# Kernel tuning notes

Hardware: AMD Instinct MI355X
Metric: run time of the kernel (lower is better)

Reference implementation:

```python
import jax, jax.numpy as jnp
import numpy as np

B, T, D, H = 2, 2048, 1024, 16
DH = D // H  # 64


def setup_inputs() -> dict:
    key = jax.random.key(0)
    k1, k2, k3 = jax.random.split(key, 3)
    x = jax.random.normal(k1, (B, T, D), dtype=jnp.float32)
    # torch nn.Linear(d, 3d, bias=False): y = x @ W.T; we store W already transposed as [in, out]
    Wqkv = jax.random.normal(k2, (D, 3 * D), dtype=jnp.float32) * (1.0 / np.sqrt(D))
    Wproj = jax.random.normal(k3, (D, D), dtype=jnp.float32) * (1.0 / np.sqrt(D))
    return {"x": x, "Wqkv": Wqkv, "Wproj": Wproj}


def reference(x, Wqkv, Wproj):
    Bx, Tx, C = x.shape
    qkv = x @ Wqkv                                   # [B,T,3C]
    q, k, v = jnp.split(qkv, 3, axis=-1)
    def rs(t):
        return t.reshape(Bx, Tx, H, DH).transpose(0, 2, 1, 3)  # [B,H,T,DH]
    q, k, v = rs(q), rs(k), rs(v)
    scale = 1.0 / jnp.sqrt(jnp.asarray(DH, dtype=x.dtype))
    att = jnp.einsum('bhqd,bhkd->bhqk', q, k) * scale          # [B,H,T,T]
    causal = jnp.tril(jnp.ones((Tx, Tx), dtype=bool))
    att = jnp.where(causal[None, None, :, :], att, jnp.asarray(-jnp.inf, dtype=att.dtype))
    att = jax.nn.softmax(att, axis=-1)
    out = jnp.einsum('bhqk,bhkd->bhqd', att, v)                # [B,H,T,DH]
    out = out.transpose(0, 2, 1, 3).reshape(Bx, Tx, C)         # [B,T,C]
    return out @ Wproj
```

## Files before the change

### kernel.cpp

```cpp
#include <hip/hip_runtime.h>
#include <hip/hip_bf16.h>

#define BB 2
#define TT 2048
#define DD 1024
#define HH 16
#define MM (BB*TT)
#define N3 (3*DD)
#define QKW 2048

typedef __attribute__((ext_vector_type(8))) short short8;
typedef __attribute__((ext_vector_type(4))) float f32x4;
typedef __attribute__((ext_vector_type(16))) float f32x16;

#define ZERO16 (f32x16){0,0,0,0,0,0,0,0,0,0,0,0,0,0,0,0}

#define GLDS16(g, l) __builtin_amdgcn_global_load_lds( \
    (const __attribute__((address_space(1))) void*)(g), \
    (__attribute__((address_space(3))) void*)(l), 16, 0, 0)

__device__ __forceinline__ unsigned short f2bf(float f) {
    union { float f; unsigned u; } v; v.f = f;
    unsigned r = v.u + 0x7FFFu + ((v.u >> 16) & 1u);
    return (unsigned short)(r >> 16);
}

__device__ __forceinline__ unsigned cvt_pk_bf16(float lo, float hi) {
    unsigned r;
    asm("v_cvt_pk_bf16_f32 %0, %1, %2" : "=v"(r) : "v"(lo), "v"(hi));
    return r;
}

__device__ __forceinline__ float fast_exp2(float x) {
    float r;
    asm("v_exp_f32 %0, %1" : "=v"(r) : "v"(x));
    return r;
}
__device__ __forceinline__ float fast_rcp(float x) {
    float r;
    asm("v_rcp_f32 %0, %1" : "=v"(r) : "v"(x));
    return r;
}

__global__ void prep_kernel(const float* __restrict__ x,
                            const float* __restrict__ Wqkv,
                            const float* __restrict__ Wproj,
                            unsigned short* __restrict__ xb,
                            unsigned short* __restrict__ wqkvt,
                            unsigned short* __restrict__ wprojt) {
    __shared__ float tile[32][33];
    const int bid = blockIdx.x;
    const int tx = threadIdx.x, ty = threadIdx.y;
    if (bid < 4096) {
        const float* src;
        unsigned short* dst;
        int rows, cols, c0, r0;
        if (bid < 3072) {
            src = Wqkv; dst = wqkvt; rows = DD; cols = N3;
            c0 = (bid % 96) * 32; r0 = (bid / 96) * 32;
        } else {
            src = Wproj; dst = wprojt; rows = DD; cols = DD;
            int b2 = bid - 3072;
            c0 = (b2 & 31) * 32; r0 = (b2 >> 5) * 32;
        }
#pragma unroll
        for (int i = 0; i < 4; i++) {
            int r = ty + i * 8;
            tile[r][tx] = src[(size_t)(r0 + r) * cols + c0 + tx];
        }
        __syncthreads();
#pragma unroll
        for (int i = 0; i < 4; i++) {
            int r = ty + i * 8;
            dst[(size_t)(c0 + r) * rows + r0 + tx] = f2bf(tile[tx][r]);
        }
    } else {
        const int t = ty * 32 + tx;
        int i = (bid - 4096) * 256 + t;
#pragma unroll
        for (int k = 0; k < 2; k++, i += 262144) {
            const float4* s = reinterpret_cast<const float4*>(x) + (size_t)i * 2;
            float4 a = s[0], b = s[1];
            unsigned short r[8] = {f2bf(a.x), f2bf(a.y), f2bf(a.z), f2bf(a.w),
                                   f2bf(b.x), f2bf(b.y), f2bf(b.z), f2bf(b.w)};
            *reinterpret_cast<uint4*>(xb + (size_t)i * 8) = *reinterpret_cast<uint4*>(r);
        }
    }
}

__global__ __launch_bounds__(512, 2)
void gemm256_qkv(const unsigned short* __restrict__ A,
                 const unsigned short* __restrict__ Bt,
                 unsigned short* __restrict__ qkv2,
                 unsigned short* __restrict__ Vout,
                 float scale) {
    __shared__ unsigned short Al[2][2][128][64];
    __shared__ unsigned short Bl[2][192][64];

    const int id = blockIdx.y * 16 + blockIdx.x;
    const int swzid = (id & 7) * 32 + (id >> 3);
    const int tm = (swzid >> 4) * 256, tn = (swzid & 15) * 192;
    const int t = threadIdx.x, w = t >> 6, l = t & 63;
    const int wm = w >> 2, wn = w & 3;
    const int lo = l & 15, hi = l >> 4;
    const int srow = l >> 3;
    const int sg = (l & 7) ^ srow;

    f32x4 acc[8][3];
#pragma unroll
    for (int i = 0; i < 8; i++)
#pragma unroll
        for (int j = 0; j < 3; j++) acc[i][j] = (f32x4){0.f, 0.f, 0.f, 0.f};

    const unsigned short* Abase = A + (size_t)(tm + w * 16 + srow) * 1024 + sg * 8;
    const unsigned short* Bbase = Bt + (size_t)(tn + w * 24 + srow) * 1024 + sg * 8;

#define STG_A(KT, H) { \
    GLDS16(Abase + (size_t)(H) * 128 * 1024 + ((KT) & 15) * 64, &Al[(KT) & 1][H][w * 16][0]); \
    GLDS16(Abase + (size_t)(H) * 128 * 1024 + 8 * 1024 + ((KT) & 15) * 64, &Al[(KT) & 1][H][w * 16 + 8][0]); }
#define STG_B(KT) { \
    GLDS16(Bbase + ((KT) & 15) * 64, &Bl[(KT) & 1][w * 24][0]); \
    GLDS16(Bbase + (size_t)8 * 1024 + ((KT) & 15) * 64, &Bl[(KT) & 1][w * 24 + 8][0]); \
    GLDS16(Bbase + (size_t)16 * 1024 + ((KT) & 15) * 64, &Bl[(KT) & 1][w * 24 + 16][0]); }

#define LOAD_A(AFR, KP, MH) { \
    const char* ab = (const char*)&Al[KP][wm][0][0]; \
    _Pragma("unroll") \
    for (int fi = 0; fi < 4; fi++) \
    _Pragma("unroll") \
    for (int ks = 0; ks < 2; ks++) \
        AFR[fi][ks] = *reinterpret_cast<const short8*>( \
            ab + ((MH) * 64 + fi * 16 + lo) * 128 + (((ks * 4 + hi) ^ (lo & 7)) << 4)); }
#define LOAD_B(BFR, KP) { \
    const char* bb = (const char*)&Bl[KP][0][0]; \
    _Pragma("unroll") \
    for (int fj = 0; fj < 3; fj++) \
    _Pragma("unroll") \
    for (int ks = 0; ks < 2; ks++) \
        BFR[fj][ks] = *reinterpret_cast<const short8*>( \
            bb + (wn * 48 + fj * 16 + lo) * 128 + (((ks * 4 + hi) ^ (lo & 7)) << 4)); }

#define MFMA24(MH, AFR, BFR) { \
    _Pragma("unroll") \
    for (int ks = 0; ks < 2; ks++) \
    _Pragma("unroll") \
    for (int fi = 0; fi < 4; fi++) \
    _Pragma("unroll") \
    for (int fj = 0; fj < 3; fj++) \
        acc[(MH) * 4 + fi][fj] = __builtin_amdgcn_mfma_f32_16x16x32_bf16( \
            AFR[fi][ks], BFR[fj][ks], acc[(MH) * 4 + fi][fj], 0, 0, 0); }

#define BAR __builtin_amdgcn_s_barrier()
#define LGKM0 asm volatile("s_waitcnt lgkmcnt(0)")
#define SP1 __builtin_amdgcn_s_setprio(1)
#define SP0 __builtin_amdgcn_s_setprio(0)

    STG_A(0, 0); STG_A(0, 1); STG_B(0); STG_B(1);
    asm volatile("s_waitcnt vmcnt(3)");
    BAR;

    for (int i = 0; i < 8; i++) {
        const int kt = 2 * i;
        short8 AF[4][2], BF[3][2];
        LOAD_A(AF, 0, 0); LOAD_B(BF, 0);
        STG_A(kt + 1, 0); STG_A(kt + 1, 1);
        BAR; LGKM0; SP1; MFMA24(0, AF, BF); SP0; BAR;
        LOAD_A(AF, 0, 1);
        STG_B(kt + 2);
        BAR; LGKM0; SP1; MFMA24(1, AF, BF); SP0;
        asm volatile("s_waitcnt vmcnt(3)");
        BAR;
        LOAD_A(AF, 1, 0); LOAD_B(BF, 1);
        STG_A(kt + 2, 0); STG_A(kt + 2, 1);
        BAR; LGKM0; SP1; MFMA24(0, AF, BF); SP0; BAR;
        LOAD_A(AF, 1, 1);
        STG_B(kt + 3);
        BAR; LGKM0; SP1; MFMA24(1, AF, BF); SP0;
        asm volatile("s_waitcnt vmcnt(3)");
        BAR;
    }

#pragma unroll
    for (int i = 0; i < 8; i++)
#pragma unroll
        for (int j = 0; j < 3; j++) {
            const int col = tn + wn * 48 + j * 16 + lo;
            const int row0 = tm + wm * 128 + i * 16 + hi * 4;
            if (col < 2 * DD) {
                float s = (col < DD) ? scale : 1.0f;
#pragma unroll
                for (int r = 0; r < 4; r++)
                    qkv2[(size_t)(row0 + r) * QKW + col] = f2bf(acc[i][j][r] * s);
            } else {
                unsigned short pk[4];
#pragma unroll
                for (int r = 0; r < 4; r++) pk[r] = f2bf(acc[i][j][r]);
                *reinterpret_cast<uint2*>(&Vout[(size_t)(col - 2 * DD) * MM + row0]) =
                    *reinterpret_cast<uint2*>(pk);
            }
        }
#undef STG_A
#undef STG_B
#undef LOAD_A
#undef LOAD_B
#undef MFMA24
#undef BAR
#undef LGKM0
#undef SP1
#undef SP0
}

__global__ __launch_bounds__(256, 4)
void gemm_proj(const unsigned short* __restrict__ A,
               const unsigned short* __restrict__ Bt,
               float* __restrict__ Cout) {
    __shared__ unsigned short As[128][64];
    __shared__ unsigned short Bs[64][64];
    const int nbx = 16;
    const int id = blockIdx.y * nbx + blockIdx.x;
    const int cpx = 512 >> 3;
    const int swz = (id & 7) * cpx + (id >> 3);
    const int tm = (swz / nbx) * 128, tn = (swz % nbx) * 64;
    const int t = threadIdx.x;
    const int w = t >> 6, lane = t & 63, lo = lane & 15, hi = lane >> 4;
    const int wr = w >> 1, wc = w & 1;

    f32x4 acc[4][2];
#pragma unroll
    for (int i = 0; i < 4; i++)
#pragma unroll
        for (int j = 0; j < 2; j++) acc[i][j] = (f32x4){0.f, 0.f, 0.f, 0.f};

    const int sr8 = lane >> 3;
    const int scol = (lane & 7) * 8;
    const unsigned short* ga = &A[(size_t)(tm + w * 32 + sr8) * 1024 + scol];
    const unsigned short* gb = &Bt[(size_t)(tn + w * 16 + sr8) * 1024 + scol];

    for (int k0 = 0; k0 < 1024; k0 += 64) {
        __syncthreads();
#pragma unroll
        for (int i = 0; i < 4; i++)
            GLDS16(ga + (size_t)(i * 8) * 1024 + k0, &As[w * 32 + i * 8][0]);
#pragma unroll
        for (int i = 0; i < 2; i++)
            GLDS16(gb + (size_t)(i * 8) * 1024 + k0, &Bs[w * 16 + i * 8][0]);
        __syncthreads();

        short8 af[4][2], bf[2][2];
#pragma unroll
        for (int i = 0; i < 4; i++)
#pragma unroll
            for (int ks = 0; ks < 2; ks++)
                af[i][ks] = *reinterpret_cast<const short8*>(&As[wr * 64 + i * 16 + lo][ks * 32 + hi * 8]);
#pragma unroll
        for (int j = 0; j < 2; j++)
#pragma unroll
            for (int ks = 0; ks < 2; ks++)
                bf[j][ks] = *reinterpret_cast<const short8*>(&Bs[wc * 32 + j * 16 + lo][ks * 32 + hi * 8]);
#pragma unroll
        for (int ks = 0; ks < 2; ks++)
#pragma unroll
            for (int i = 0; i < 4; i++)
#pragma unroll
                for (int j = 0; j < 2; j++)
                    acc[i][j] = __builtin_amdgcn_mfma_f32_16x16x32_bf16(af[i][ks], bf[j][ks], acc[i][j], 0, 0, 0);
    }
#pragma unroll
    for (int i = 0; i < 4; i++)
#pragma unroll
        for (int j = 0; j < 2; j++) {
            const int col = tn + wc * 32 + j * 16 + lo;
            const int row0 = tm + wr * 64 + i * 16 + hi * 4;
#pragma unroll
            for (int r = 0; r < 4; r++)
                Cout[(size_t)(row0 + r) * DD + col] = acc[i][j][r];
        }
}

struct AttnState {
    f32x16 o0, o1, lD;
};

__device__ __forceinline__ void attn_full_tile(
        const char* kbase, const char* vbase, const short8* bq, short8 ones1,
        AttnState& st, int sw4, int ql, int hi8, bool domask, int kvb, int qg) {
    short8 ak0[4], ak1[4];
#pragma unroll
    for (int ks = 0; ks < 4; ks++) {
        ak0[ks] = *reinterpret_cast<const short8*>(kbase + ql * 128 + (((ks * 2 + hi8) << 4) ^ sw4));
        ak1[ks] = *reinterpret_cast<const short8*>(kbase + (32 + ql) * 128 + (((ks * 2 + hi8) << 4) ^ sw4));
    }
    f32x16 sa0 = ZERO16, sa1 = ZERO16;
    __builtin_amdgcn_s_setprio(1);
#pragma unroll
    for (int ks = 0; ks < 4; ks++) {
        sa0 = __builtin_amdgcn_mfma_f32_32x32x16_bf16(ak0[ks], bq[ks], sa0, 0, 0, 0);
        sa1 = __builtin_amdgcn_mfma_f32_32x32x16_bf16(ak1[ks], bq[ks], sa1, 0, 0, 0);
    }
    __builtin_amdgcn_s_setprio(0);
    if (domask) {
#pragma unroll
        for (int r = 0; r < 16; r++) {
            int crow = (r & 3) + 8 * (r >> 2) + 4 * hi8;
            if (kvb + crow > qg) sa0[r] = -1e30f;
            if (kvb + 32 + crow > qg) sa1[r] = -1e30f;
        }
    }
#pragma unroll
    for (int r = 0; r < 16; r++) sa0[r] = fast_exp2(sa0[r]);
#pragma unroll
    for (int r = 0; r < 16; r++) sa1[r] = fast_exp2(sa1[r]);

    unsigned a01 = cvt_pk_bf16(sa0[0], sa0[1]),  a23 = cvt_pk_bf16(sa0[2], sa0[3]);
    unsigned a45 = cvt_pk_bf16(sa0[4], sa0[5]),  a67 = cvt_pk_bf16(sa0[6], sa0[7]);
    asm("v_permlane32_swap_b32 %0, %1" : "+v"(a01), "+v"(a45));
    asm("v_permlane32_swap_b32 %0, %1" : "+v"(a23), "+v"(a67));
    unsigned b01 = cvt_pk_bf16(sa0[8], sa0[9]),  b23 = cvt_pk_bf16(sa0[10], sa0[11]);
    unsigned b45 = cvt_pk_bf16(sa0[12], sa0[13]), b67 = cvt_pk_bf16(sa0[14], sa0[15]);
    asm("v_permlane32_swap_b32 %0, %1" : "+v"(b01), "+v"(b45));
    asm("v_permlane32_swap_b32 %0, %1" : "+v"(b23), "+v"(b67));
    unsigned c01 = cvt_pk_bf16(sa1[0], sa1[1]),  c23 = cvt_pk_bf16(sa1[2], sa1[3]);
    unsigned c45 = cvt_pk_bf16(sa1[4], sa1[5]),  c67 = cvt_pk_bf16(sa1[6], sa1[7]);
    asm("v_permlane32_swap_b32 %0, %1" : "+v"(c01), "+v"(c45));
    asm("v_permlane32_swap_b32 %0, %1" : "+v"(c23), "+v"(c67));
    unsigned d01 = cvt_pk_bf16(sa1[8], sa1[9]),  d23 = cvt_pk_bf16(sa1[10], sa1[11]);
    unsigned d45 = cvt_pk_bf16(sa1[12], sa1[13]), d67 = cvt_pk_bf16(sa1[14], sa1[15]);
    asm("v_permlane32_swap_b32 %0, %1" : "+v"(d01), "+v"(d45));
    asm("v_permlane32_swap_b32 %0, %1" : "+v"(d23), "+v"(d67));
    union { unsigned u[4]; short8 s; } f0s0, f1s0, f0s1, f1s1;
    f0s0.u[0] = a01; f0s0.u[1] = a23; f0s0.u[2] = a45; f0s0.u[3] = a67;
    f1s0.u[0] = b01; f1s0.u[1] = b23; f1s0.u[2] = b45; f1s0.u[3] = b67;
    f0s1.u[0] = c01; f0s1.u[1] = c23; f0s1.u[2] = c45; f0s1.u[3] = c67;
    f1s1.u[0] = d01; f1s1.u[1] = d23; f1s1.u[2] = d45; f1s1.u[3] = d67;

    short8 bv00 = *reinterpret_cast<const short8*>(vbase + ql * 128 + (((0 + hi8) << 4) ^ sw4));
    short8 bv01 = *reinterpret_cast<const short8*>(vbase + ql * 128 + (((2 + hi8) << 4) ^ sw4));
    short8 bv02 = *reinterpret_cast<const short8*>(vbase + ql * 128 + (((4 + hi8) << 4) ^ sw4));
    short8 bv03 = *reinterpret_cast<const short8*>(vbase + ql * 128 + (((6 + hi8) << 4) ^ sw4));
    short8 bv10 = *reinterpret_cast<const short8*>(vbase + (32 + ql) * 128 + (((0 + hi8) << 4) ^ sw4));
    short8 bv11 = *reinterpret_cast<const short8*>(vbase + (32 + ql) * 128 + (((2 + hi8) << 4) ^ sw4));
    short8 bv12 = *reinterpret_cast<const short8*>(vbase + (32 + ql) * 128 + (((4 + hi8) << 4) ^ sw4));
    short8 bv13 = *reinterpret_cast<const short8*>(vbase + (32 + ql) * 128 + (((6 + hi8) << 4) ^ sw4));
    __builtin_amdgcn_s_setprio(1);
    st.lD = __builtin_amdgcn_mfma_f32_32x32x16_bf16(f0s0.s, ones1, st.lD, 0, 0, 0);
    st.lD = __builtin_amdgcn_mfma_f32_32x32x16_bf16(f1s0.s, ones1, st.lD, 0, 0, 0);
    st.lD = __builtin_amdgcn_mfma_f32_32x32x16_bf16(f0s1.s, ones1, st.lD, 0, 0, 0);
    st.lD = __builtin_amdgcn_mfma_f32_32x32x16_bf16(f1s1.s, ones1, st.lD, 0, 0, 0);
    st.o0 = __builtin_amdgcn_mfma_f32_32x32x16_bf16(f0s0.s, bv00, st.o0, 0, 0, 0);
    st.o1 = __builtin_amdgcn_mfma_f32_32x32x16_bf16(f0s0.s, bv10, st.o1, 0, 0, 0);
    st.o0 = __builtin_amdgcn_mfma_f32_32x32x16_bf16(f1s0.s, bv01, st.o0, 0, 0, 0);
    st.o1 = __builtin_amdgcn_mfma_f32_32x32x16_bf16(f1s0.s, bv11, st.o1, 0, 0, 0);
    st.o0 = __builtin_amdgcn_mfma_f32_32x32x16_bf16(f0s1.s, bv02, st.o0, 0, 0, 0);
    st.o1 = __builtin_amdgcn_mfma_f32_32x32x16_bf16(f0s1.s, bv12, st.o1, 0, 0, 0);
    st.o0 = __builtin_amdgcn_mfma_f32_32x32x16_bf16(f1s1.s, bv03, st.o0, 0, 0, 0);
    st.o1 = __builtin_amdgcn_mfma_f32_32x32x16_bf16(f1s1.s, bv13, st.o1, 0, 0, 0);
    __builtin_amdgcn_s_setprio(0);
}

__device__ __forceinline__ void attn_half_tile(
        const char* kbase, const char* vbase, const short8* bq, short8 ones1,
        AttnState& st, int sw4, int ql, int hi8, int sub, int kvb, int qg) {
    short8 ak[4];
#pragma unroll
    for (int ks = 0; ks < 4; ks++)
        ak[ks] = *reinterpret_cast<const short8*>(
            kbase + (sub * 32 + ql) * 128 + (((ks * 2 + hi8) << 4) ^ sw4));
    f32x16 sa = ZERO16;
#pragma unroll
    for (int ks = 0; ks < 4; ks++)
        sa = __builtin_amdgcn_mfma_f32_32x32x16_bf16(ak[ks], bq[ks], sa, 0, 0, 0);

#pragma unroll
    for (int r = 0; r < 16; r++) {
        int crow = (r & 3) + 8 * (r >> 2) + 4 * hi8;
        if (kvb + sub * 32 + crow > qg) sa[r] = -1e30f;
    }
#pragma unroll
    for (int r = 0; r < 16; r++) sa[r] = fast_exp2(sa[r]);

    unsigned a01 = cvt_pk_bf16(sa[0], sa[1]),  a23 = cvt_pk_bf16(sa[2], sa[3]);
    unsigned a45 = cvt_pk_bf16(sa[4], sa[5]),  a67 = cvt_pk_bf16(sa[6], sa[7]);
    asm("v_permlane32_swap_b32 %0, %1" : "+v"(a01), "+v"(a45));
    asm("v_permlane32_swap_b32 %0, %1" : "+v"(a23), "+v"(a67));
    unsigned b01 = cvt_pk_bf16(sa[8], sa[9]),  b23 = cvt_pk_bf16(sa[10], sa[11]);
    unsigned b45 = cvt_pk_bf16(sa[12], sa[13]), b67 = cvt_pk_bf16(sa[14], sa[15]);
    asm("v_permlane32_swap_b32 %0, %1" : "+v"(b01), "+v"(b45));
    asm("v_permlane32_swap_b32 %0, %1" : "+v"(b23), "+v"(b67));
    union { unsigned u[4]; short8 s; } f0, f1;
    f0.u[0] = a01; f0.u[1] = a23; f0.u[2] = a45; f0.u[3] = a67;
    f1.u[0] = b01; f1.u[1] = b23; f1.u[2] = b45; f1.u[3] = b67;

    st.lD = __builtin_amdgcn_mfma_f32_32x32x16_bf16(f0.s, ones1, st.lD, 0, 0, 0);
    st.lD = __builtin_amdgcn_mfma_f32_32x32x16_bf16(f1.s, ones1, st.lD, 0, 0, 0);

    short8 bv00 = *reinterpret_cast<const short8*>(vbase + ql * 128 + (((sub * 4 + 0 + hi8) << 4) ^ sw4));
    short8 bv01 = *reinterpret_cast<const short8*>(vbase + ql * 128 + (((sub * 4 + 2 + hi8) << 4) ^ sw4));
    short8 bv10 = *reinterpret_cast<const short8*>(vbase + (32 + ql) * 128 + (((sub * 4 + 0 + hi8) << 4) ^ sw4));
    short8 bv11 = *reinterpret_cast<const short8*>(vbase + (32 + ql) * 128 + (((sub * 4 + 2 + hi8) << 4) ^ sw4));
    st.o0 = __builtin_amdgcn_mfma_f32_32x32x16_bf16(f0.s, bv00, st.o0, 0, 0, 0);
    st.o1 = __builtin_amdgcn_mfma_f32_32x32x16_bf16(f0.s, bv10, st.o1, 0, 0, 0);
    st.o0 = __builtin_amdgcn_mfma_f32_32x32x16_bf16(f1.s, bv01, st.o0, 0, 0, 0);
    st.o1 = __builtin_amdgcn_mfma_f32_32x32x16_bf16(f1.s, bv11, st.o1, 0, 0, 0);
}

__global__ __launch_bounds__(256)
void attn_kernel(const unsigned short* __restrict__ qkv2,
                 const unsigned short* __restrict__ vtg,
                 unsigned short* __restrict__ outp) {
    __shared__ unsigned short Ks[4][64][64];
    __shared__ unsigned short Vt[4][64][64];

    const int b = blockIdx.z, h = blockIdx.x, p = blockIdx.y;
    const int qcl = p, qch = 31 - p;
    const int L = p + 1, Hn = 32 - p;
    const int NSTEP = 17;
    const int t = threadIdx.x;
    const int w = t >> 6, l = t & 63, ql = l & 31, hi8 = l >> 5;
    const int pr = w >> 1, rg = w & 1;
    const int q0h = qch * 64 + rg * 32;
    const int q0l = qcl * 64 + rg * 32;
    const int q0p = pr ? q0l : q0h;
    const unsigned short* base2 = qkv2 + (size_t)b * TT * QKW;

    short8 bq[4];
#pragma unroll
    for (int ks = 0; ks < 4; ks++)
        bq[ks] = *reinterpret_cast<const short8*>(
            &base2[(size_t)(q0p + ql) * QKW + h * 64 + ks * 16 + hi8 * 8]);

    AttnState st;
    st.o0 = ZERO16; st.o1 = ZERO16; st.lD = ZERO16;

    short8 ones1;
#pragma unroll
    for (int j = 0; j < 8; j++) ones1[j] = (short)0x3F80;

    const int krow = l >> 3;
    const int kc8 = (l & 7) ^ krow;
    const unsigned short* gk = &base2[(size_t)(w * 8 + krow) * QKW + DD + h * 64 + kc8 * 8];
    const unsigned short* gv = &vtg[(size_t)(h * 64 + w * 8 + krow) * MM + b * TT + kc8 * 8];

#define STAGE(TI) { \
    const int _s = (TI) & 3; \
    const size_t _kb = (size_t)(TI) * 64; \
    GLDS16(gk + _kb * QKW, &Ks[_s][w * 8][0]); \
    GLDS16(gk + (_kb + 32) * QKW, &Ks[_s][32 + w * 8][0]); \
    GLDS16(gv + _kb, &Vt[_s][w * 8][0]); \
    GLDS16(gv + (size_t)32 * MM + _kb, &Vt[_s][32 + w * 8][0]); }

#define WRITE_OUT(Q0) { \
    _Pragma("unroll") \
    for (int r = 0; r < 16; r++) { \
        int src = (r & 3) + 8 * (r >> 2) + 4 * hi8; \
        float inv = fast_rcp(st.lD[r]); \
        size_t off = (size_t)(b * TT + (Q0) + src) * DD + h * 64 + ql; \
        outp[off] = f2bf(st.o0[r] * inv); \
        outp[off + 32] = f2bf(st.o1[r] * inv); \
    } }

    STAGE(0);
    int nIss = 1;
    __syncthreads();

    const int sw4 = (ql & 7) << 4;
    for (int s = 0; s < NSTEP; s++) {
        {
            const int sn = s + 1;
            int lastN;
            if (sn < L) lastN = sn;
            else if (sn < NSTEP - 1) lastN = L + 2 * (sn - L) + 1;
            else if (sn == NSTEP - 1) lastN = Hn - 1;
            else lastN = -1;
            while (nIss <= lastN) { STAGE(nIss); nIss++; }
        }

        if (s == L && pr == 1) {
            WRITE_OUT(q0l);
            st.o0 = ZERO16; st.o1 = ZERO16; st.lD = ZERO16;
#pragma unroll
            for (int ks = 0; ks < 4; ks++)
                bq[ks] = *reinterpret_cast<const short8*>(
                    &base2[(size_t)(q0h + ql) * QKW + h * 64 + ks * 16 + hi8 * 8]);
        }

        if (s < L) {
            const int tile = s;
            const char* kbase = (const char*)&Ks[tile & 3][0][0];
            const char* vbase = (const char*)&Vt[tile & 3][0][0];
            const bool domask = (pr == 1) && (s == L - 1);
            attn_full_tile(kbase, vbase, bq, ones1, st, sw4, ql, hi8,
                           domask, tile * 64, q0p + ql);
        } else if (s < NSTEP - 1) {
            const int tile = L + 2 * (s - L) + pr;
            const char* kbase = (const char*)&Ks[tile & 3][0][0];
            const char* vbase = (const char*)&Vt[tile & 3][0][0];
            attn_full_tile(kbase, vbase, bq, ones1, st, sw4, ql, hi8,
                           false, 0, 0);
        } else {
            const int tile = Hn - 1;
            const char* kbase = (const char*)&Ks[tile & 3][0][0];
            const char* vbase = (const char*)&Vt[tile & 3][0][0];
            attn_half_tile(kbase, vbase, bq, ones1, st, sw4, ql, hi8,
                           pr, tile * 64, q0h + ql);
        }
        __syncthreads();
    }

    float* xf = (float*)&Ks[0][0][0];
    float* xl = (float*)&Vt[0][0][0];
    const int tid128 = (w & 1) * 64 + l;
    if (pr == 1) {
#pragma unroll
        for (int r = 0; r < 16; r++) {
            xf[r * 128 + tid128] = st.o0[r];
            xf[(16 + r) * 128 + tid128] = st.o1[r];
            xl[r * 128 + tid128] = st.lD[r];
        }
    }
    __syncthreads();
    if (pr == 0) {
#pragma unroll
        for (int r = 0; r < 16; r++) {
            st.o0[r] += xf[r * 128 + tid128];
            st.o1[r] += xf[(16 + r) * 128 + tid128];
            st.lD[r] += xl[r * 128 + tid128];
        }
        WRITE_OUT(q0h);
    }
#undef STAGE
#undef WRITE_OUT
}

extern "C" void kernel_launch(void* const* d_in, const int* in_sizes, int n_in,
                              void* d_out, int out_size, void* d_ws, size_t ws_size,
                              hipStream_t stream) {
    const float* x     = (const float*)d_in[0];
    const float* Wqkv  = (const float*)d_in[1];
    const float* Wproj = (const float*)d_in[2];
    float* out = (float*)d_out;

    unsigned short* xb     = (unsigned short*)d_ws;
    unsigned short* wqkvt  = xb + (size_t)MM * DD;
    unsigned short* wprojt = wqkvt + (size_t)N3 * DD;
    unsigned short* qkv2   = wprojt + (size_t)DD * DD;
    unsigned short* vtg    = qkv2 + (size_t)MM * QKW;
    unsigned short* attout = vtg + (size_t)DD * MM;
    size_t need = ((size_t)MM * DD + (size_t)N3 * DD + (size_t)DD * DD +
                   (size_t)MM * QKW + (size_t)DD * MM + (size_t)MM * DD) * 2;
    if (ws_size < need) return;

    const float sc = 0.125f * 1.44269504088896f;

    prep_kernel<<<5120, dim3(32, 8), 0, stream>>>(x, Wqkv, Wproj, xb, wqkvt, wprojt);

    gemm256_qkv<<<dim3(16, 16), 512, 0, stream>>>(xb, wqkvt, qkv2, vtg, sc);

    attn_kernel<<<dim3(HH, 16, BB), 256, 0, stream>>>(qkv2, vtg, attout);

    gemm_proj<<<dim3(16, 32), 256, 0, stream>>>(attout, wprojt, out);
}
```

Before: 101.2 us.

## Defer PV MFMAs one step to overlap with next tile's QK and softmax

Software-pipelines the attention inner loop. Each step now saves its bf16 probabilities and V fragments into a pending struct instead of running the P·V and row-sum MFMAs right away. Those deferred MFMAs are issued in the next step, right after that step's QK MFMAs and under raised priority, so matrix work can overlap the exp and pack VALU work. Pending work is flushed before the mid-loop output write and in the final half tile. The pending struct holds about 48 more VGPRs, which risks lower occupancy or register spills.

Result: slower. 118.2 us (+16.8%).

```diff
diff --git a/kernel.cpp b/kernel.cpp
--- a/kernel.cpp
+++ b/kernel.cpp
@@ -280,10 +280,30 @@
 struct AttnState {
     f32x16 o0, o1, lD;
 };
-
-__device__ __forceinline__ void attn_full_tile(
+struct Pend {
+    short8 f0, f1, f2, f3;
+    short8 bv00, bv01, bv02, bv03, bv10, bv11, bv12, bv13;
+};
+
+__device__ __forceinline__ void flush_pv(Pend& pd, AttnState& st, short8 ones1) {
+    st.lD = __builtin_amdgcn_mfma_f32_32x32x16_bf16(pd.f0, ones1, st.lD, 0, 0, 0);
+    st.lD = __builtin_amdgcn_mfma_f32_32x32x16_bf16(pd.f1, ones1, st.lD, 0, 0, 0);
+    st.lD = __builtin_amdgcn_mfma_f32_32x32x16_bf16(pd.f2, ones1, st.lD, 0, 0, 0);
+    st.lD = __builtin_amdgcn_mfma_f32_32x32x16_bf16(pd.f3, ones1, st.lD, 0, 0, 0);
+    st.o0 = __builtin_amdgcn_mfma_f32_32x32x16_bf16(pd.f0, pd.bv00, st.o0, 0, 0, 0);
+    st.o1 = __builtin_amdgcn_mfma_f32_32x32x16_bf16(pd.f0, pd.bv10, st.o1, 0, 0, 0);
+    st.o0 = __builtin_amdgcn_mfma_f32_32x32x16_bf16(pd.f1, pd.bv01, st.o0, 0, 0, 0);
+    st.o1 = __builtin_amdgcn_mfma_f32_32x32x16_bf16(pd.f1, pd.bv11, st.o1, 0, 0, 0);
+    st.o0 = __builtin_amdgcn_mfma_f32_32x32x16_bf16(pd.f2, pd.bv02, st.o0, 0, 0, 0);
+    st.o1 = __builtin_amdgcn_mfma_f32_32x32x16_bf16(pd.f2, pd.bv12, st.o1, 0, 0, 0);
+    st.o0 = __builtin_amdgcn_mfma_f32_32x32x16_bf16(pd.f3, pd.bv03, st.o0, 0, 0, 0);
+    st.o1 = __builtin_amdgcn_mfma_f32_32x32x16_bf16(pd.f3, pd.bv13, st.o1, 0, 0, 0);
+}
+
+__device__ __forceinline__ void attn_step_full(
         const char* kbase, const char* vbase, const short8* bq, short8 ones1,
-        AttnState& st, int sw4, int ql, int hi8, bool domask, int kvb, int qg) {
+        AttnState& st, Pend& pd, bool pvalid,
+        int sw4, int ql, int hi8, bool domask, int kvb, int qg) {
     short8 ak0[4], ak1[4];
 #pragma unroll
     for (int ks = 0; ks < 4; ks++) {
@@ -297,7 +317,9 @@
         sa0 = __builtin_amdgcn_mfma_f32_32x32x16_bf16(ak0[ks], bq[ks], sa0, 0, 0, 0);
         sa1 = __builtin_amdgcn_mfma_f32_32x32x16_bf16(ak1[ks], bq[ks], sa1, 0, 0, 0);
     }
+    if (pvalid) flush_pv(pd, st, ones1);
     __builtin_amdgcn_s_setprio(0);
+
     if (domask) {
 #pragma unroll
         for (int r = 0; r < 16; r++) {
@@ -327,48 +349,39 @@
     unsigned d45 = cvt_pk_bf16(sa1[12], sa1[13]), d67 = cvt_pk_bf16(sa1[14], sa1[15]);
     asm("v_permlane32_swap_b32 %0, %1" : "+v"(d01), "+v"(d45));
     asm("v_permlane32_swap_b32 %0, %1" : "+v"(d23), "+v"(d67));
-    union { unsigned u[4]; short8 s; } f0s0, f1s0, f0s1, f1s1;
-    f0s0.u[0] = a01; f0s0.u[1] = a23; f0s0.u[2] = a45; f0s0.u[3] = a67;
-    f1s0.u[0] = b01; f1s0.u[1] = b23; f1s0.u[2] = b45; f1s0.u[3] = b67;
-    f0s1.u[0] = c01; f0s1.u[1] = c23; f0s1.u[2] = c45; f0s1.u[3] = c67;
-    f1s1.u[0] = d01; f1s1.u[1] = d23; f1s1.u[2] = d45; f1s1.u[3] = d67;
-
-    short8 bv00 = *reinterpret_cast<const short8*>(vbase + ql * 128 + (((0 + hi8) << 4) ^ sw4));
-    short8 bv01 = *reinterpret_cast<const short8*>(vbase + ql * 128 + (((2 + hi8) << 4) ^ sw4));
-    short8 bv02 = *reinterpret_cast<const short8*>(vbase + ql * 128 + (((4 + hi8) << 4) ^ sw4));
-    short8 bv03 = *reinterpret_cast<const short8*>(vbase + ql * 128 + (((6 + hi8) << 4) ^ sw4));
-    short8 bv10 = *reinterpret_cast<const short8*>(vbase + (32 + ql) * 128 + (((0 + hi8) << 4) ^ sw4));
-    short8 bv11 = *reinterpret_cast<const short8*>(vbase + (32 + ql) * 128 + (((2 + hi8) << 4) ^ sw4));
-    short8 bv12 = *reinterpret_cast<const short8*>(vbase + (32 + ql) * 128 + (((4 + hi8) << 4) ^ sw4));
-    short8 bv13 = *reinterpret_cast<const short8*>(vbase + (32 + ql) * 128 + (((6 + hi8) << 4) ^ sw4));
-    __builtin_amdgcn_s_setprio(1);
-    st.lD = __builtin_amdgcn_mfma_f32_32x32x16_bf16(f0s0.s, ones1, st.lD, 0, 0, 0);
-    st.lD = __builtin_amdgcn_mfma_f32_32x32x16_bf16(f1s0.s, ones1, st.lD, 0, 0, 0);
-    st.lD = __builtin_amdgcn_mfma_f32_32x32x16_bf16(f0s1.s, ones1, st.lD, 0, 0, 0);
-    st.lD = __builtin_amdgcn_mfma_f32_32x32x16_bf16(f1s1.s, ones1, st.lD, 0, 0, 0);
-    st.o0 = __builtin_amdgcn_mfma_f32_32x32x16_bf16(f0s0.s, bv00, st.o0, 0, 0, 0);
-    st.o1 = __builtin_amdgcn_mfma_f32_32x32x16_bf16(f0s0.s, bv10, st.o1, 0, 0, 0);
-    st.o0 = __builtin_amdgcn_mfma_f32_32x32x16_bf16(f1s0.s, bv01, st.o0, 0, 0, 0);
-    st.o1 = __builtin_amdgcn_mfma_f32_32x32x16_bf16(f1s0.s, bv11, st.o1, 0, 0, 0);
-    st.o0 = __builtin_amdgcn_mfma_f32_32x32x16_bf16(f0s1.s, bv02, st.o0, 0, 0, 0);
-    st.o1 = __builtin_amdgcn_mfma_f32_32x32x16_bf16(f0s1.s, bv12, st.o1, 0, 0, 0);
-    st.o0 = __builtin_amdgcn_mfma_f32_32x32x16_bf16(f1s1.s, bv03, st.o0, 0, 0, 0);
-    st.o1 = __builtin_amdgcn_mfma_f32_32x32x16_bf16(f1s1.s, bv13, st.o1, 0, 0, 0);
-    __builtin_amdgcn_s_setprio(0);
-}
-
-__device__ __forceinline__ void attn_half_tile(
+    union { unsigned u[4]; short8 s; } u0, u1, u2, u3;
+    u0.u[0] = a01; u0.u[1] = a23; u0.u[2] = a45; u0.u[3] = a67;
+    u1.u[0] = b01; u1.u[1] = b23; u1.u[2] = b45; u1.u[3] = b67;
+    u2.u[0] = c01; u2.u[1] = c23; u2.u[2] = c45; u2.u[3] = c67;
+    u3.u[0] = d01; u3.u[1] = d23; u3.u[2] = d45; u3.u[3] = d67;
+    pd.f0 = u0.s; pd.f1 = u1.s; pd.f2 = u2.s; pd.f3 = u3.s;
+
+    pd.bv00 = *reinterpret_cast<const short8*>(vbase + ql * 128 + (((0 + hi8) << 4) ^ sw4));
+    pd.bv01 = *reinterpret_cast<const short8*>(vbase + ql * 128 + (((2 + hi8) << 4) ^ sw4));
+    pd.bv02 = *reinterpret_cast<const short8*>(vbase + ql * 128 + (((4 + hi8) << 4) ^ sw4));
+    pd.bv03 = *reinterpret_cast<const short8*>(vbase + ql * 128 + (((6 + hi8) << 4) ^ sw4));
+    pd.bv10 = *reinterpret_cast<const short8*>(vbase + (32 + ql) * 128 + (((0 + hi8) << 4) ^ sw4));
+    pd.bv11 = *reinterpret_cast<const short8*>(vbase + (32 + ql) * 128 + (((2 + hi8) << 4) ^ sw4));
+    pd.bv12 = *reinterpret_cast<const short8*>(vbase + (32 + ql) * 128 + (((4 + hi8) << 4) ^ sw4));
+    pd.bv13 = *reinterpret_cast<const short8*>(vbase + (32 + ql) * 128 + (((6 + hi8) << 4) ^ sw4));
+}
+
+__device__ __forceinline__ void attn_step_half(
         const char* kbase, const char* vbase, const short8* bq, short8 ones1,
-        AttnState& st, int sw4, int ql, int hi8, int sub, int kvb, int qg) {
+        AttnState& st, Pend& pd, bool pvalid,
+        int sw4, int ql, int hi8, int sub, int kvb, int qg) {
     short8 ak[4];
 #pragma unroll
     for (int ks = 0; ks < 4; ks++)
         ak[ks] = *reinterpret_cast<const short8*>(
             kbase + (sub * 32 + ql) * 128 + (((ks * 2 + hi8) << 4) ^ sw4));
     f32x16 sa = ZERO16;
+    __builtin_amdgcn_s_setprio(1);
 #pragma unroll
     for (int ks = 0; ks < 4; ks++)
         sa = __builtin_amdgcn_mfma_f32_32x32x16_bf16(ak[ks], bq[ks], sa, 0, 0, 0);
+    if (pvalid) flush_pv(pd, st, ones1);
+    __builtin_amdgcn_s_setprio(0);
 
 #pragma unroll
     for (int r = 0; r < 16; r++) {
@@ -430,6 +443,8 @@
 
     AttnState st;
     st.o0 = ZERO16; st.o1 = ZERO16; st.lD = ZERO16;
+    Pend pend;
+    bool pvalid = false;
 
     short8 ones1;
 #pragma unroll
@@ -475,6 +490,7 @@
         }
 
         if (s == L && pr == 1) {
+            if (pvalid) { flush_pv(pend, st, ones1); pvalid = false; }
             WRITE_OUT(q0l);
             st.o0 = ZERO16; st.o1 = ZERO16; st.lD = ZERO16;
 #pragma unroll
@@ -488,20 +504,23 @@
             const char* kbase = (const char*)&Ks[tile & 3][0][0];
             const char* vbase = (const char*)&Vt[tile & 3][0][0];
             const bool domask = (pr == 1) && (s == L - 1);
-            attn_full_tile(kbase, vbase, bq, ones1, st, sw4, ql, hi8,
+            attn_step_full(kbase, vbase, bq, ones1, st, pend, pvalid, sw4, ql, hi8,
                            domask, tile * 64, q0p + ql);
+            pvalid = true;
         } else if (s < NSTEP - 1) {
             const int tile = L + 2 * (s - L) + pr;
             const char* kbase = (const char*)&Ks[tile & 3][0][0];
             const char* vbase = (const char*)&Vt[tile & 3][0][0];
-            attn_full_tile(kbase, vbase, bq, ones1, st, sw4, ql, hi8,
+            attn_step_full(kbase, vbase, bq, ones1, st, pend, pvalid, sw4, ql, hi8,
                            false, 0, 0);
+            pvalid = true;
         } else {
             const int tile = Hn - 1;
             const char* kbase = (const char*)&Ks[tile & 3][0][0];
             const char* vbase = (const char*)&Vt[tile & 3][0][0];
-            attn_half_tile(kbase, vbase, bq, ones1, st, sw4, ql, hi8,
+            attn_step_half(kbase, vbase, bq, ones1, st, pend, pvalid, sw4, ql, hi8,
                            pr, tile * 64, q0h + ql);
+            pvalid = false;
         }
         __syncthreads();
     }
```
